# Kernel optimization log

Measured on AMD Instinct MI355X. Metric: run time of the kernel, lower is better.

Reference implementation:

```python
import jax, jax.numpy as jnp
import numpy as np

B, S, E = 1, 2048, 2048
H = 16            # num_q_heads
DN = 128          # qk_nope_head_dim
DR = 64           # qk_rope_head_dim
DV = 128          # v_head_dim
R = 512           # kv_lora_rank
QLR = 1536        # q_lora_rank
EPS = 1e-6
ROPE_BASE = 10000.0


def _rmsnorm(x, w):
    var = jnp.mean(jnp.square(x), axis=-1, keepdims=True)
    return x * jax.lax.rsqrt(var + EPS) * w


def _rope_cos_sin(seqlen):
    inv_freq = 1.0 / (ROPE_BASE ** (jnp.arange(0, DR, 2, dtype=jnp.float32) / DR))
    ang = jnp.arange(seqlen, dtype=jnp.float32)[:, None] * inv_freq[None, :]  # [S, DR/2]
    cos = jnp.concatenate([jnp.cos(ang), jnp.cos(ang)], axis=-1)  # [S, DR]
    sin = jnp.concatenate([jnp.sin(ang), jnp.sin(ang)], axis=-1)
    return cos, sin


def _rotate_half(x):
    x1, x2 = jnp.split(x, 2, axis=-1)
    return jnp.concatenate([-x2, x1], axis=-1)


def setup_inputs() -> dict:
    key = jax.random.key(0)
    ks = jax.random.split(key, 8)
    sd = lambda fan_in: 1.0 / np.sqrt(fan_in)
    return {
        "x": jax.random.normal(ks[0], (B, S, E), jnp.float32),
        "w_q_a": jax.random.normal(ks[1], (E, QLR), jnp.float32) * sd(E),
        "q_a_ln_w": jnp.ones((QLR,), jnp.float32),
        "w_q_b": jax.random.normal(ks[2], (QLR, H * (DN + DR)), jnp.float32) * sd(QLR),
        "w_kv_a": jax.random.normal(ks[3], (E, R + DR), jnp.float32) * sd(E),
        "kv_a_ln_w": jnp.ones((R,), jnp.float32),
        "w_kv_b": jax.random.normal(ks[4], (R, H * (DN + DV)), jnp.float32) * sd(R),
        "w_o": jax.random.normal(ks[5], (H * DV, E), jnp.float32) * sd(H * DV),
    }


def reference(x, w_q_a, q_a_ln_w, w_q_b, w_kv_a, kv_a_ln_w, w_kv_b, w_o):
    b, s, _ = x.shape
    # --- low-rank query projection: q_a -> RMSNorm -> q_b ---
    q_a = _rmsnorm(x @ w_q_a, q_a_ln_w)                      # [b,s,QLR]
    q = (q_a @ w_q_b).reshape(b, s, H, DN + DR)               # [b,s,H,192]
    q_nope, q_pe = q[..., :DN], q[..., DN:]
    # --- compressed KV projection (MQA, single KV head) ---
    ckv_kpe = x @ w_kv_a                                      # [b,s,R+DR]
    ckv = _rmsnorm(ckv_kpe[..., :R], kv_a_ln_w)               # [b,s,R]
    k_pe = ckv_kpe[..., R:].reshape(b, s, 1, DR)              # [b,s,1,DR]
    # --- partial RoPE on the rope sub-dims only ---
    cos, sin = _rope_cos_sin(s)
    cos, sin = cos[None, :, None, :], sin[None, :, None, :]
    q_pe = q_pe * cos + _rotate_half(q_pe) * sin
    k_pe = k_pe * cos + _rotate_half(k_pe) * sin
    # --- weight absorption: fold W_uk into q, W_uv @ W_o into output ---
    w_kv = w_kv_b.reshape(R, H, DN + DV)
    w_uk = w_kv[..., :DN]                                     # [R,H,DN]
    w_uv = w_kv[..., DN:]                                     # [R,H,DV]
    w_o3 = w_o.reshape(H, DV, E)
    w_o_abs = jnp.einsum('rhd,hde->hre', w_uv, w_o3)          # [H,R,E]
    q_abs = jnp.einsum('bshd,rhd->bshr', q_nope, w_uk)        # [b,s,H,R]
    # --- attention in compressed (ckv + rope) space ---
    q_full = jnp.concatenate([q_abs, q_pe], axis=-1)          # [b,s,H,R+DR]
    k_full = jnp.concatenate([ckv, k_pe[:, :, 0, :]], axis=-1)  # [b,s,R+DR]
    sm_scale = (DN + DR) ** -0.5
    scores = jnp.einsum('bqhd,bkd->bhqk', q_full, k_full) * sm_scale
    causal = jnp.tril(jnp.ones((s, s), dtype=bool))
    scores = jnp.where(causal[None, None], scores, jnp.finfo(scores.dtype).min)
    attn = jax.nn.softmax(scores, axis=-1)
    o_ckv = jnp.einsum('bhqk,bkr->bqhr', attn, ckv)           # [b,s,H,R]
    # --- absorbed output projection, summed over heads ---
    y = jnp.einsum('bqhr,hre->bqe', o_ckv, w_o_abs)           # [b,s,E]
    return y
```

## Files before the change

kernel.cpp:

```cpp
#include <hip/hip_runtime.h>
#include <math.h>


typedef unsigned short u16;
typedef unsigned int u32;
typedef __bf16 bf16x8 __attribute__((ext_vector_type(8)));
typedef float f32x4 __attribute__((ext_vector_type(4)));
typedef unsigned short u16x8 __attribute__((ext_vector_type(8)));

__device__ __forceinline__ u16 f2b(float f) {
  u32 u = __float_as_uint(f);
  u += 0x7FFFu + ((u >> 16) & 1u);
  return (u16)(u >> 16);
}
__device__ __forceinline__ float b2f(u16 v) {
  return __uint_as_float(((u32)v) << 16);
}

#define GLDS(g, l) __builtin_amdgcn_global_load_lds( \
    (const __attribute__((address_space(1))) u32*)(g), \
    (__attribute__((address_space(3))) u32*)(l), 16, 0, 0)

#define MFMA(a, b, c) __builtin_amdgcn_mfma_f32_16x16x32_bf16(a, b, c, 0, 0, 0)

template<int N>
__device__ __forceinline__ void vm_barrier() {
  __builtin_amdgcn_s_waitcnt(0xF70 | N);
  __builtin_amdgcn_s_barrier();
}

#define N_ITEMS_G 160
__device__ __forceinline__ int nkc_of(int qt) { return (((qt >> 1) + 1) + 3) >> 2; }

__device__ __forceinline__ float block_sum(float v, float* red) {
#pragma unroll
  for (int off = 32; off > 0; off >>= 1) v += __shfl_down(v, off);
  const int lane = threadIdx.x & 63, w = threadIdx.x >> 6;
  if (lane == 0) red[w] = v;
  __syncthreads();
  float r = red[0] + red[1] + red[2] + red[3];
  __syncthreads();
  return r;
}

template<int OUTK>
__global__ __launch_bounds__(256) void gemm_mfma(
    const u16* __restrict__ A, const u16* __restrict__ B, void* __restrict__ Cv,
    int K, int lda, int ldb, int ldc, long sA, long sB, long sC)
{
  __shared__ u16 At[3][4096];
  __shared__ u16 Bt[3][4096];
  const u16* Ab = A + (long)blockIdx.z * sA;
  const u16* Bb = B + (long)blockIdx.z * sB;
  const int tid = threadIdx.x;
  const int w = tid >> 6, lane = tid & 63;
  const int m0 = blockIdx.y * 128, n0 = blockIdx.x * 128;
  const int wm = (w >> 1) * 64, wn = (w & 1) * 64;
  const int fr = lane & 15, fq = lane >> 4;

  const int c0 = w * 2, c1 = w * 2 + 1;
  const int e0 = (c0 * 64 + lane) * 8, e1 = (c1 * 64 + lane) * 8;
  const int r0 = e0 >> 5, col0 = e0 & 31;
  const int r1 = e1 >> 5, col1 = e1 & 31;

  const int nk = K >> 5;
  auto issue = [&](int kc) {
    const int k0 = kc * 32;
    u16* at = At[kc % 3];
    u16* bt = Bt[kc % 3];
    GLDS(Ab + (long)(m0 + r0) * lda + k0 + col0, at + c0 * 512);
    GLDS(Bb + (long)(n0 + r0) * ldb + k0 + col0, bt + c0 * 512);
    GLDS(Ab + (long)(m0 + r1) * lda + k0 + col1, at + c1 * 512);
    GLDS(Bb + (long)(n0 + r1) * ldb + k0 + col1, bt + c1 * 512);
  };

  f32x4 acc[4][4] = {};
  issue(0);
  issue(1);
  vm_barrier<4>();
  for (int kc = 0; kc < nk; ++kc) {
    if (kc + 2 < nk) issue(kc + 2);
    const u16* at = At[kc % 3];
    const u16* bt = Bt[kc % 3];
    bf16x8 af[4], bfr[4];
#pragma unroll
    for (int i = 0; i < 4; ++i)
      af[i] = *(const bf16x8*)(at + (wm + i * 16 + fr) * 32 + fq * 8);
#pragma unroll
    for (int j = 0; j < 4; ++j)
      bfr[j] = *(const bf16x8*)(bt + (wn + j * 16 + fr) * 32 + fq * 8);
#pragma unroll
    for (int i = 0; i < 4; ++i)
#pragma unroll
      for (int j = 0; j < 4; ++j)
        acc[i][j] = MFMA(af[i], bfr[j], acc[i][j]);
    if (kc + 1 < nk) {
      if (kc + 2 < nk) vm_barrier<4>();
      else vm_barrier<0>();
    }
  }

  if (OUTK == 0) {
    float* C = (float*)Cv + (long)blockIdx.z * sC;
#pragma unroll
    for (int i = 0; i < 4; ++i)
#pragma unroll
      for (int j = 0; j < 4; ++j) {
        long base = (long)(m0 + wm + i * 16 + fq * 4) * ldc + (n0 + wn + j * 16 + fr);
#pragma unroll
        for (int r = 0; r < 4; ++r) C[base + (long)r * ldc] = acc[i][j][r];
      }
  } else if (OUTK == 1) {
    u16* C = (u16*)Cv + (long)blockIdx.z * sC;
#pragma unroll
    for (int i = 0; i < 4; ++i)
#pragma unroll
      for (int j = 0; j < 4; ++j) {
        long base = (long)(m0 + wm + i * 16 + fq * 4) * ldc + (n0 + wn + j * 16 + fr);
#pragma unroll
        for (int r = 0; r < 4; ++r) C[base + (long)r * ldc] = f2b(acc[i][j][r]);
      }
  } else {
    u16* C = (u16*)Cv + (long)blockIdx.z * sC;
#pragma unroll
    for (int i = 0; i < 4; ++i)
#pragma unroll
      for (int j = 0; j < 4; ++j) {
        ushort4 v = { f2b(acc[i][j][0]), f2b(acc[i][j][1]),
                      f2b(acc[i][j][2]), f2b(acc[i][j][3]) };
        *(ushort4*)(C + (long)(n0 + wn + j * 16 + fr) * ldc + (m0 + wm + i * 16 + fq * 4)) = v;
      }
  }
}

__global__ void init_ctr(u32* ctr) {
  if (threadIdx.x < 8) ctr[threadIdx.x] = 0;
}

__global__ __launch_bounds__(256, 2) void attn_partial(
    const u16* __restrict__ qfb,
    const u16* __restrict__ kfb,
    const u16* __restrict__ vallT,
    u32* __restrict__ ctr,
    u16* __restrict__ pO,
    float* __restrict__ pS)
{
  __shared__ u16 Ks[3][4096];
  __shared__ u16 Ps[4 * 2176];
  __shared__ u32 cur;

  const int tid = threadIdx.x;
  const int w = tid >> 6, lane = tid & 63;
  const int fr = lane & 15, fq = lane >> 4;
  const float scale = 0.07216878364870323f;
  const int grp = (int)(blockIdx.x & 7);
  u16* Psw = Ps + w * 2176;

  const int krow0 = (w * 2) * 16 + (lane >> 2);
  const int krow1 = (w * 2 + 1) * 16 + (lane >> 2);
  const int kg0 = (lane & 3) ^ (krow0 & 3);
  const int kg1 = (lane & 3) ^ (krow1 & 3);

  while (true) {
    if (tid == 0) cur = atomicAdd(&ctr[grp], 1u);
    __syncthreads();
    const u32 it = cur;
    if (it >= N_ITEMS_G) break;

    int rem = (int)it, qt = 31, kc = 0, hh = 0;
    for (int q = 31; q >= 0; --q) {
      int cnt = nkc_of(q) * 2;
      if (rem < cnt) { qt = q; kc = rem >> 1; hh = rem & 1; break; }
      rem -= cnt;
    }
    const int h = grp + hh * 8;
    const u32 gslot = (u32)grp * N_ITEMS_G + it;
    const int q0 = qt * 64;
    const int ktt = (qt >> 1) + 1;
    const int kt0 = kc * 4, kt1 = min(kt0 + 4, ktt);

    bf16x8 aq[18];
    {
      const u16* qp = qfb + (long)(q0 + w * 16 + fr) * 9216 + h * 576 + fq * 8;
#pragma unroll
      for (int d = 0; d < 18; ++d) aq[d] = *(const bf16x8*)(qp + d * 32);
    }

    float m_run[4], l_run[4];
#pragma unroll
    for (int r = 0; r < 4; ++r) { m_run[r] = -1e30f; l_run[r] = 0.f; }
    f32x4 Oacc[8] = {};
    const u16* vlane = vallT + (long)h * 262144 + (long)fr * 2048 + fq * 8;

    auto issueK = [&](int kt, int c) {
      const int k0i = kt * 128, d0 = c * 32;
      u16* dst = Ks[c % 3];
      GLDS(kfb + (long)(k0i + krow0) * 576 + d0 + kg0 * 8, dst + (w * 2) * 512);
      GLDS(kfb + (long)(k0i + krow1) * 576 + d0 + kg1 * 8, dst + (w * 2 + 1) * 512);
    };

    issueK(kt0, 0);
    issueK(kt0, 1);

    for (int kt = kt0; kt < kt1; ++kt) {
      const int k0 = kt * 128;
      vm_barrier<2>();

      f32x4 sc[8] = {};
#pragma unroll
      for (int d = 0; d < 18; ++d) {
        if (d + 2 < 18) issueK(kt, d + 2);
        const u16* kb = Ks[d % 3];
        __builtin_amdgcn_s_setprio(1);
#pragma unroll
        for (int j = 0; j < 8; ++j) {
          const int row = j * 16 + fr;
          bf16x8 b = *(const bf16x8*)(kb + row * 32 + ((fq ^ (row & 3)) * 8));
          sc[j] = MFMA(aq[d], b, sc[j]);
        }
        __builtin_amdgcn_s_setprio(0);
        if (d < 17) {
          if (d + 2 < 18) vm_barrier<2>();
          else vm_barrier<0>();
        }
      }
      __builtin_amdgcn_s_barrier();

      const u16* vk = vlane + k0;
      bf16x8 vA[4], vB[4];
#pragma unroll
      for (int q = 0; q < 4; ++q) {
        vA[q] = *(const bf16x8*)(vk + (long)q * 32768);
        vB[q] = *(const bf16x8*)(vk + (long)(q + 4) * 32768);
      }
      if (kt + 1 < kt1) { issueK(kt + 1, 0); issueK(kt + 1, 1); }

      const bool diag = (kt == ktt - 1);
#pragma unroll
      for (int r = 0; r < 4; ++r) {
        float mx = m_run[r];
#pragma unroll
        for (int j = 0; j < 8; ++j) {
          float s = sc[j][r] * scale;
          if (diag) {
            const int row = q0 + w * 16 + fq * 4 + r;
            const int col = k0 + j * 16 + fr;
            if (col > row) s = -1e30f;
          }
          sc[j][r] = s;
          mx = fmaxf(mx, s);
        }
        mx = fmaxf(mx, __shfl_xor(mx, 1));
        mx = fmaxf(mx, __shfl_xor(mx, 2));
        mx = fmaxf(mx, __shfl_xor(mx, 4));
        mx = fmaxf(mx, __shfl_xor(mx, 8));
        const float alpha = __expf(m_run[r] - mx);
        m_run[r] = mx;
        float sum = 0.f;
#pragma unroll
        for (int j = 0; j < 8; ++j) {
          float p = __expf(sc[j][r] - mx);
          sc[j][r] = p;
          sum += p;
        }
        sum += __shfl_xor(sum, 1);
        sum += __shfl_xor(sum, 2);
        sum += __shfl_xor(sum, 4);
        sum += __shfl_xor(sum, 8);
        l_run[r] = l_run[r] * alpha + sum;
#pragma unroll
        for (int jv = 0; jv < 8; ++jv) Oacc[jv][r] *= alpha;
#pragma unroll
        for (int j = 0; j < 8; ++j)
          Psw[(fq * 4 + r) * 136 + j * 16 + fr] = f2b(sc[j][r]);
      }

#pragma unroll
      for (int ks = 0; ks < 4; ++ks) {
        bf16x8 ap = *(const bf16x8*)(Psw + fr * 136 + ks * 32 + fq * 8);
        __builtin_amdgcn_s_setprio(1);
#pragma unroll
        for (int q = 0; q < 4; ++q) Oacc[q] = MFMA(ap, vA[q], Oacc[q]);
        __builtin_amdgcn_s_setprio(0);
        if (ks < 3) {
#pragma unroll
          for (int q = 0; q < 4; ++q)
            vA[q] = *(const bf16x8*)(vk + (long)q * 32768 + (ks + 1) * 32);
        }
        __builtin_amdgcn_s_setprio(1);
#pragma unroll
        for (int q = 0; q < 4; ++q) Oacc[q + 4] = MFMA(ap, vB[q], Oacc[q + 4]);
        __builtin_amdgcn_s_setprio(0);
        if (ks < 3) {
#pragma unroll
          for (int q = 0; q < 4; ++q)
            vB[q] = *(const bf16x8*)(vk + (long)(q + 4) * 32768 + (ks + 1) * 32);
        }
      }
    }

    const long po = (long)gslot * 8192;
#pragma unroll
    for (int r = 0; r < 4; ++r) {
      const int lr = w * 16 + fq * 4 + r;
      if (fr == 0) {
        pS[((long)gslot * 64 + lr) * 2] = m_run[r];
        pS[((long)gslot * 64 + lr) * 2 + 1] = l_run[r];
      }
#pragma unroll
      for (int jv = 0; jv < 8; ++jv)
        pO[po + (long)lr * 128 + jv * 16 + fr] = f2b(Oacc[jv][r]);
    }
  }
}

__global__ __launch_bounds__(256) void attn_reduce(
    const u16* __restrict__ pO, const float* __restrict__ pS,
    u16* __restrict__ ovb)
{
  const int h = blockIdx.x, qt = blockIdx.y;
  const int g = h & 7, hh = h >> 3;
  const int ktt = (qt >> 1) + 1;
  const int nkc = (ktt + 3) >> 2;
  int base = g * N_ITEMS_G;
  for (int q = qt + 1; q < 32; ++q) base += nkc_of(q) * 2;
  const int tid = threadIdx.x;
  const int r = tid >> 2, cq = (tid & 3) * 32;

  float m[4], l[4], wgt[4];
  float M = -1e30f;
  for (int i = 0; i < nkc; ++i) {
    const long slot = base + i * 2 + hh;
    m[i] = pS[(slot * 64 + r) * 2];
    l[i] = pS[(slot * 64 + r) * 2 + 1];
    M = fmaxf(M, m[i]);
  }
  float L = 0.f;
  for (int i = 0; i < nkc; ++i) { wgt[i] = __expf(m[i] - M); L += l[i] * wgt[i]; }
  const float inv = 1.0f / L;

  u16* orow = ovb + (long)(qt * 64 + r) * 2048 + h * 128 + cq;
  for (int c8 = 0; c8 < 32; c8 += 8) {
    float acc[8] = {};
    for (int i = 0; i < nkc; ++i) {
      const long slot = base + i * 2 + hh;
      const u16x8 v = *(const u16x8*)(pO + (slot * 64 + r) * 128 + cq + c8);
#pragma unroll
      for (int e = 0; e < 8; ++e) acc[e] += b2f(v[e]) * wgt[i];
    }
    u16x8 o;
#pragma unroll
    for (int e = 0; e < 8; ++e) o[e] = f2b(acc[e] * inv);
    *(u16x8*)(orow + c8) = o;
  }
}

__global__ __launch_bounds__(256) void cast_bf16(const float* __restrict__ in,
                                                 u16* __restrict__ out, long n) {
  long i = ((long)blockIdx.x * 256 + threadIdx.x) * 4;
  if (i >= n) return;
  float4 v = *(const float4*)(in + i);
  ushort4 o = { f2b(v.x), f2b(v.y), f2b(v.z), f2b(v.w) };
  *(ushort4*)(out + i) = o;
}

__global__ __launch_bounds__(256) void transpose_cast(const float* __restrict__ in,
    u16* __restrict__ out, int ldi, int ldo, long sIn, long sOut) {
  in += (long)blockIdx.z * sIn;
  out += (long)blockIdx.z * sOut;
  __shared__ u16 t[32][33];
  const int i0 = blockIdx.y * 32, j0 = blockIdx.x * 32;
  const int tx = threadIdx.x & 31, ty = threadIdx.x >> 5;
  for (int r = ty; r < 32; r += 8)
    t[r][tx] = f2b(in[(long)(i0 + r) * ldi + j0 + tx]);
  __syncthreads();
  for (int r = ty; r < 32; r += 8)
    out[(long)(j0 + r) * ldo + i0 + tx] = t[tx][r];
}

__global__ __launch_bounds__(256) void rmsnorm_cast(const float* __restrict__ in,
    const float* __restrict__ w, u16* __restrict__ out, int n, int ldin) {
  __shared__ float red[4];
  const float* row = in + (long)blockIdx.x * ldin;
  u16* orow = out + (long)blockIdx.x * n;
  float ss = 0.f;
  for (int i = threadIdx.x; i < n; i += 256) { float v = row[i]; ss += v * v; }
  float tot = block_sum(ss, red);
  float inv = rsqrtf(tot / (float)n + 1e-6f);
  for (int i = threadIdx.x; i < n; i += 256) orow[i] = f2b(row[i] * inv * w[i]);
}

__global__ __launch_bounds__(256) void rope_table(float* tab) {
  int s = blockIdx.x * 8 + (threadIdx.x >> 5), j = threadIdx.x & 31;
  double freq = pow(10000.0, -(double)j / 32.0);
  double ang = (double)s * freq;
  tab[s * 64 + j] = (float)cos(ang);
  tab[s * 64 + 32 + j] = (float)sin(ang);
}

__global__ __launch_bounds__(256) void build_kfull(const float* __restrict__ ckv,
    const float* __restrict__ lnw, const float* __restrict__ tab, u16* __restrict__ kfb) {
  __shared__ float red[4];
  const int s = blockIdx.x;
  const float* row = ckv + (long)s * 2176;
  float ss = 0.f;
  for (int i = threadIdx.x; i < 512; i += 256) { float v = row[i]; ss += v * v; }
  float tot = block_sum(ss, red);
  float inv = rsqrtf(tot / 512.0f + 1e-6f);
  u16* orow = kfb + (long)s * 576;
  for (int i = threadIdx.x; i < 512; i += 256) orow[i] = f2b(row[i] * inv * lnw[i]);
  if (threadIdx.x < 64) {
    int i = threadIdx.x, j = i & 31;
    float c = tab[s * 64 + j], sn = tab[s * 64 + 32 + j];
    float xv = row[512 + i];
    float rot = (i < 32) ? -row[512 + i + 32] : row[512 + i - 32];
    orow[512 + i] = f2b(xv * c + rot * sn);
  }
}

__global__ __launch_bounds__(256) void rope_qpe(const u16* __restrict__ qb,
    const float* __restrict__ tab, u16* __restrict__ qfb) {
  const int s = blockIdx.x;
  const int h = threadIdx.x >> 4;
  const int i0 = (threadIdx.x & 15) * 4;
  const u16* src = qb + (long)s * 3072 + h * 192 + 128;
  u16* dst = qfb + (long)s * 9216 + h * 576 + 512;
#pragma unroll
  for (int k = 0; k < 4; ++k) {
    const int i = i0 + k, j = i & 31;
    float c = tab[s * 64 + j], sn = tab[s * 64 + 32 + j];
    float xv = b2f(src[i]);
    float rot = (i < 32) ? -b2f(src[i + 32]) : b2f(src[i - 32]);
    dst[i] = f2b(xv * c + rot * sn);
  }
}

extern "C" void kernel_launch(void* const* d_in, const int* in_sizes, int n_in,
                              void* d_out, int out_size, void* d_ws, size_t ws_size,
                              hipStream_t stream) {
  const float* x      = (const float*)d_in[0];
  const float* w_q_a  = (const float*)d_in[1];
  const float* q_ln   = (const float*)d_in[2];
  const float* w_q_b  = (const float*)d_in[3];
  const float* w_kv_a = (const float*)d_in[4];
  const float* kv_ln  = (const float*)d_in[5];
  const float* w_kv_b = (const float*)d_in[6];
  const float* w_o    = (const float*)d_in[7];
  float* out = (float*)d_out;

  char* p = (char*)d_ws;
  float* tab   = (float*)p;  p += 524288;
  u16* wkvbb   = (u16*)p;    p += 4194304;
  u16* wuvT    = (u16*)p;    p += 2097152;
  u16* woT     = (u16*)p;    p += 8388608;
  u16* qfb     = (u16*)p;    p += 37748736;
  u16* vallT   = (u16*)p;    p += 8388608;
  u16* kfb     = (u16*)p;    p += 2359296;
  u16* ovb     = (u16*)p;    p += 8388608;
  char* tb = p;
  u16* xb      = (u16*)tb;
  u16* wabT    = (u16*)(tb + 8388608);
  float* qac   = (float*)(tb + 17301504);
  u16* qab     = (u16*)(tb + 35127296);
  u16* wqbT    = (u16*)(tb + 41418752);
  u16* qb      = (u16*)(tb + 50855936);
  u16* pO      = (u16*)tb;
  float* pS    = (float*)(tb + 20971520);
  u32* ctr     = (u32*)(tb + 21626880);

  rope_table<<<dim3(256), 256, 0, stream>>>(tab);

  cast_bf16<<<4096, 256, 0, stream>>>(x, xb, 4194304);
  transpose_cast<<<dim3(48, 64), 256, 0, stream>>>(w_q_a, wabT, 1536, 2048, 0, 0);
  transpose_cast<<<dim3(18, 64), 256, 0, stream>>>(w_kv_a, wabT + 1536 * 2048, 576, 2048, 0, 0);
  transpose_cast<<<dim3(96, 48), 256, 0, stream>>>(w_q_b, wqbT, 3072, 1536, 0, 0);
  cast_bf16<<<2048, 256, 0, stream>>>(w_kv_b, wkvbb, 2097152);
  transpose_cast<<<dim3(4, 16, 16), 256, 0, stream>>>(w_kv_b + 128, wuvT, 4096, 512, 256, 65536);
  transpose_cast<<<dim3(64, 64), 256, 0, stream>>>(w_o, woT, 2048, 2048, 0, 0);

  gemm_mfma<0><<<dim3(17, 16), 256, 0, stream>>>(
      xb, wabT, qac, 2048, 2048, 2048, 2176, 0, 0, 0);
  rmsnorm_cast<<<2048, 256, 0, stream>>>(qac, q_ln, qab, 1536, 2176);
  build_kfull<<<2048, 256, 0, stream>>>(qac + 1536, kv_ln, tab, kfb);

  gemm_mfma<1><<<dim3(24, 16), 256, 0, stream>>>(
      qab, wqbT, qb, 1536, 1536, 1536, 3072, 0, 0, 0);

  gemm_mfma<1><<<dim3(4, 16, 16), 256, 0, stream>>>(
      qb, wkvbb, qfb, 128, 3072, 4096, 9216, 192, 256, 576);
  rope_qpe<<<dim3(2048), 256, 0, stream>>>(qb, tab, qfb);

  gemm_mfma<2><<<dim3(1, 16, 16), 256, 0, stream>>>(
      kfb, wuvT, vallT, 512, 576, 512, 2048, 0, 65536, 262144);

  init_ctr<<<1, 64, 0, stream>>>(ctr);
  attn_partial<<<dim3(768), 256, 0, stream>>>(qfb, kfb, vallT, ctr, pO, pS);
  attn_reduce<<<dim3(16, 32), 256, 0, stream>>>(pO, pS, ovb);

  gemm_mfma<0><<<dim3(16, 16), 256, 0, stream>>>(
      ovb, woT, out, 2048, 2048, 2048, 2048, 0, 0, 0);
}
```

Baseline: 508.3 us.

## Double K-chunk granularity and prefetch next tile's K inside the score loop

The K staging buffer grows from three 32-wide chunks to three 64-wide chunk groups, so each pipeline stage loads two chunks and runs 16 MFMAs between barriers instead of 8. The prefetch of the next key tile's first two groups now happens inside the last iterations of the score loop rather than after it, which removes the trailing block barrier. This halves the number of vm barriers per tile and overlaps the next tile's loads with the current tile's score work. In exchange it doubles LDS use for K, which may lower occupancy under the 2-blocks-per-CU launch bound, and dropping the s_barrier risks a race on reused buffers.

```diff
diff --git a/kernel.cpp b/kernel.cpp
--- a/kernel.cpp
+++ b/kernel.cpp
@@ -145,7 +145,7 @@
     u16* __restrict__ pO,
     float* __restrict__ pS)
 {
-  __shared__ u16 Ks[3][4096];
+  __shared__ u16 Ks[3 * 8192];
   __shared__ u16 Ps[4 * 2176];
   __shared__ u32 cur;
 
@@ -192,39 +192,47 @@
     f32x4 Oacc[8] = {};
     const u16* vlane = vallT + (long)h * 262144 + (long)fr * 2048 + fq * 8;
 
-    auto issueK = [&](int kt, int c) {
-      const int k0i = kt * 128, d0 = c * 32;
-      u16* dst = Ks[c % 3];
-      GLDS(kfb + (long)(k0i + krow0) * 576 + d0 + kg0 * 8, dst + (w * 2) * 512);
-      GLDS(kfb + (long)(k0i + krow1) * 576 + d0 + kg1 * 8, dst + (w * 2 + 1) * 512);
+    auto issueG = [&](int kt, int gk, int gb) {
+      const int k0i = kt * 128;
+      u16* buf = Ks + gb * 8192;
+#pragma unroll
+      for (int c = 0; c < 2; ++c) {
+        const int d0 = (gk * 2 + c) * 32;
+        u16* dst = buf + c * 4096;
+        GLDS(kfb + (long)(k0i + krow0) * 576 + d0 + kg0 * 8, dst + (w * 2) * 512);
+        GLDS(kfb + (long)(k0i + krow1) * 576 + d0 + kg1 * 8, dst + (w * 2 + 1) * 512);
+      }
     };
 
-    issueK(kt0, 0);
-    issueK(kt0, 1);
+    issueG(kt0, 0, 0);
+    issueG(kt0, 1, 1);
 
     for (int kt = kt0; kt < kt1; ++kt) {
       const int k0 = kt * 128;
-      vm_barrier<2>();
+      vm_barrier<4>();
 
       f32x4 sc[8] = {};
 #pragma unroll
-      for (int d = 0; d < 18; ++d) {
-        if (d + 2 < 18) issueK(kt, d + 2);
-        const u16* kb = Ks[d % 3];
+      for (int g = 0; g < 9; ++g) {
+        const int gg = g + 2;
+        if (gg <= 8) issueG(kt, gg, gg % 3);
+        else if (kt + 1 < kt1) issueG(kt + 1, gg - 9, gg % 3);
+        const u16* kb0 = Ks + (g % 3) * 8192;
         __builtin_amdgcn_s_setprio(1);
 #pragma unroll
-        for (int j = 0; j < 8; ++j) {
-          const int row = j * 16 + fr;
-          bf16x8 b = *(const bf16x8*)(kb + row * 32 + ((fq ^ (row & 3)) * 8));
-          sc[j] = MFMA(aq[d], b, sc[j]);
+        for (int c = 0; c < 2; ++c) {
+          const int d = 2 * g + c;
+          const u16* kb = kb0 + c * 4096;
+#pragma unroll
+          for (int j = 0; j < 8; ++j) {
+            const int row = j * 16 + fr;
+            bf16x8 b = *(const bf16x8*)(kb + row * 32 + ((fq ^ (row & 3)) * 8));
+            sc[j] = MFMA(aq[d], b, sc[j]);
+          }
         }
         __builtin_amdgcn_s_setprio(0);
-        if (d < 17) {
-          if (d + 2 < 18) vm_barrier<2>();
-          else vm_barrier<0>();
-        }
-      }
-      __builtin_amdgcn_s_barrier();
+        if (g < 8) vm_barrier<4>();
+      }
 
       const u16* vk = vlane + k0;
       bf16x8 vA[4], vB[4];
@@ -233,7 +241,6 @@
         vA[q] = *(const bf16x8*)(vk + (long)q * 32768);
         vB[q] = *(const bf16x8*)(vk + (long)(q + 4) * 32768);
       }
-      if (kt + 1 < kt1) { issueK(kt + 1, 0); issueK(kt + 1, 1); }
 
       const bool diag = (kt == ktt - 1);
 #pragma unroll
```

Result: no change. 499.0 us (-1.8%).
